# Performance work log

Measured on AMD Instinct MI355X. Metric: run time of the kernel, lower is better.

## Reference

```python
import jax, jax.numpy as jnp
import numpy as np
from jax import lax

B, T = 8, 256
GRID = (8, 8, 8)
X, Y, Z = GRID
N = X * Y * Z            # 512 nodes
C_IN = C_OUT = 8         # 4096 / 512
R = 8                    # num_rand


def _stencil_mask():
    # 7-point stencil mask at kernel center (1,1,1)
    m = np.zeros((3, 3, 3), dtype=np.float32)
    c = 1
    m[c, c, c] = 1.0
    m[c - 1, c, c] = 1.0
    m[c + 1, c, c] = 1.0
    m[c, c - 1, c] = 1.0
    m[c, c + 1, c] = 1.0
    m[c, c, c - 1] = 1.0
    m[c, c, c + 1] = 1.0
    return jnp.asarray(m)


def setup_inputs() -> dict:
    key = jax.random.key(0)
    k1, k2, k3, k4 = jax.random.split(key, 4)
    x = jax.random.normal(k1, (B, T, C_IN * N), dtype=jnp.float32)
    # MaskedConv3d params (kernel 3x3x3)
    fan = C_IN * 27
    conv_w = jax.random.normal(k2, (C_OUT, C_IN, 3, 3, 3), dtype=jnp.float32) / np.sqrt(fan)
    conv_b = jnp.zeros((C_OUT,), dtype=jnp.float32)
    # RandomGraphMixer3D params (xavier-uniform-like)
    bound = np.sqrt(6.0 / (C_IN * R + C_OUT))
    mix_w = jax.random.uniform(k3, (C_OUT, C_IN, R), jnp.float32, -bound, bound)
    mix_b = jnp.zeros((C_OUT,), dtype=jnp.float32)
    rand_indices = jax.random.randint(k4, (N, R), 0, N, dtype=jnp.int32)
    alpha = jnp.float32(0.5)
    return {"x": x, "conv_w": conv_w, "conv_b": conv_b,
            "mix_w": mix_w, "mix_b": mix_b, "alpha": alpha,
            "rand_indices": rand_indices}


def reference(x, conv_w, conv_b, mix_w, mix_b, alpha, rand_indices):
    Bd, Td, D = x.shape
    xt = x.reshape(Bd * Td, C_IN, X, Y, Z)
    # --- masked 7-point stencil conv3d ---
    w = conv_w * _stencil_mask()  # broadcast over (O, I)
    y_local = lax.conv_general_dilated(
        xt, w, window_strides=(1, 1, 1), padding='SAME',
        dimension_numbers=('NCDHW', 'OIDHW', 'NCDHW'))
    y_local = y_local + conv_b[None, :, None, None, None]
    # --- random graph mixer: gather + contract ---
    x_nodes = xt.reshape(Bd * Td, C_IN, N)
    gathered = x_nodes[:, :, rand_indices]              # [BT, C, N, R]
    y_rand = jnp.einsum('ocr,bcnr->bon', mix_w, gathered) + mix_b[None, :, None]
    y_rand = y_rand.reshape(Bd * Td, C_OUT, X, Y, Z)
    # --- sigmoid blend ---
    a = jax.nn.sigmoid(alpha)
    yt = a * y_local + (1.0 - a) * y_rand
    return yt.reshape(Bd, Td, C_OUT * N)
```

## Files before the change

kernel.cpp:

```cpp
#include <hip/hip_runtime.h>
#include <math.h>

#define NNODES 512
#define CIN 8
#define COUT 8
#define RR 8
#define BTB 2
#define GUARD 64
#define SLOTS (GUARD + NNODES + GUARD)
#define SLAB_HW (SLOTS * 8)
#define LDS_HW (BTB * SLAB_HW)
#define WTAB 1024

typedef __attribute__((ext_vector_type(8))) short short8;
typedef __attribute__((ext_vector_type(4))) float floatx4;

__device__ __forceinline__ unsigned int pack_bf16(float a, float b) {
    unsigned int ua = __float_as_uint(a);
    unsigned int ub = __float_as_uint(b);
    ua = (ua + 0x7fffu + ((ua >> 16) & 1u)) >> 16;
    ub = (ub + 0x7fffu + ((ub >> 16) & 1u)) & 0xffff0000u;
    return ua | ub;
}

__global__ void prep(const float* __restrict__ conv_w,
                     const float* __restrict__ conv_b,
                     const float* __restrict__ mix_w,
                     const float* __restrict__ mix_b,
                     const float* __restrict__ alpha_p,
                     const int*   __restrict__ rand_idx,
                     float* __restrict__ ws) {
    const int t = threadIdx.x;
    const float a = 1.0f / (1.0f + expf(-alpha_p[0]));
    if (t < 960) {
        const int oc = t / 15;
        const int tap = t % 15;
        float v;
        if (tap < 7) {
            const int off[7] = {13, 4, 22, 10, 16, 12, 14};
            v = a * conv_w[oc * 27 + off[tap]];
        } else {
            v = (1.0f - a) * mix_w[oc * RR + (tap - 7)];
        }
        ws[t] = v;
    } else if (t < 968) {
        const int o = t - 960;
        ws[960 + o] = a * conv_b[o] + (1.0f - a) * mix_b[o];
    }

    int4* tab = (int4*)((int*)ws + WTAB);
    for (int e = t; e < 2048; e += 1024) {
        const int tt = e >> 6, lane = e & 63;
        const int q = lane >> 4, r16 = lane & 15;
        const int m = tt * 16 + r16;
        const int h = (m >> 3) & 7, w = m & 7;
        int off[4];
#pragma unroll
        for (int i = 0; i < 4; ++i) {
            const int tap = 4 * i + q;
            int o;
            if (tap == 0)       o = GUARD + m;
            else if (tap == 1)  o = GUARD + m - 64;
            else if (tap == 2)  o = GUARD + m + 64;
            else if (tap == 3)  o = (h > 0) ? (GUARD + m - 8) : 0;
            else if (tap == 4)  o = (h < 7) ? (GUARD + m + 8) : 0;
            else if (tap == 5)  o = (w > 0) ? (GUARD + m - 1) : 0;
            else if (tap == 6)  o = (w < 7) ? (GUARD + m + 1) : 0;
            else if (tap <= 14) o = GUARD + rand_idx[m * RR + (tap - 7)];
            else                o = 0;
            off[i] = o * 16;
        }
        tab[e] = make_int4(off[0], off[1], off[2], off[3]);
    }
}

__global__ __launch_bounds__(256) void hybrid3d_v3(
    const float* __restrict__ x,
    const float* __restrict__ wsb,
    float* __restrict__ out)
{
    __shared__ unsigned short lds16[LDS_HW];
    const int tid  = threadIdx.x;
    const int wave = tid >> 6;
    const int lane = tid & 63;
    const int quad = lane >> 4;
    const int r16  = lane & 15;
    const int btl  = wave >> 1;
    const int half = wave & 1;

    {
        const int b = tid >> 7;
        const int s = tid & 127;
        const int slot = (s < GUARD) ? s : (NNODES + s);
        *(uint4*)&lds16[b * SLAB_HW + slot * 8] = make_uint4(0u, 0u, 0u, 0u);
    }

    short8 bfrag[4];
#pragma unroll
    for (int i = 0; i < 4; ++i) {
        const int tap = 4 * i + quad;
        union { unsigned int u[4]; short8 s; } bf;
#pragma unroll
        for (int jp = 0; jp < 4; ++jp) {
            const int c0 = 2 * jp, c1 = 2 * jp + 1;
            float f0 = (r16 < 8 && tap < 15) ? wsb[(r16 * CIN + c0) * 15 + tap] : 0.0f;
            float f1 = (r16 < 8 && tap < 15) ? wsb[(r16 * CIN + c1) * 15 + tap] : 0.0f;
            bf.u[jp] = pack_bf16(f0, f1);
        }
        bfrag[i] = bf.s;
    }
    const float bias = (r16 < 8) ? wsb[960 + r16] : 0.0f;

    const float* xg = x + ((size_t)blockIdx.x * BTB + btl) * (CIN * NNODES);
    unsigned short* slab = lds16 + btl * SLAB_HW;
#pragma unroll
    for (int j = 0; j < 4; ++j) {
        const int n = half * 256 + j * 64 + lane;
        float v[8];
#pragma unroll
        for (int c = 0; c < 8; ++c) v[c] = xg[c * NNODES + n];
        uint4 pk;
        pk.x = pack_bf16(v[0], v[1]);
        pk.y = pack_bf16(v[2], v[3]);
        pk.z = pack_bf16(v[4], v[5]);
        pk.w = pack_bf16(v[6], v[7]);
        *(uint4*)&slab[(GUARD + n) * 8] = pk;
    }
    __syncthreads();

    const char* slabp = (const char*)slab;
    const int4* tab = (const int4*)((const int*)wsb + WTAB);
    float* outb = out + ((size_t)blockIdx.x * BTB + btl) * (COUT * NNODES);

#pragma unroll 2
    for (int tt = 0; tt < 16; ++tt) {
        const int t = half * 16 + tt;
        const int4 off = tab[t * 64 + lane];
        union { uint4 u; short8 s; } r0, r1, r2, r3;
        r0.u = *(const uint4*)(slabp + off.x);
        r1.u = *(const uint4*)(slabp + off.y);
        r2.u = *(const uint4*)(slabp + off.z);
        r3.u = *(const uint4*)(slabp + off.w);

        floatx4 acc_a = {bias, bias, bias, bias};
        floatx4 acc_b = {0.0f, 0.0f, 0.0f, 0.0f};
        acc_a = __builtin_amdgcn_mfma_f32_16x16x32_bf16(r0.s, bfrag[0], acc_a, 0, 0, 0);
        acc_b = __builtin_amdgcn_mfma_f32_16x16x32_bf16(r2.s, bfrag[2], acc_b, 0, 0, 0);
        acc_a = __builtin_amdgcn_mfma_f32_16x16x32_bf16(r1.s, bfrag[1], acc_a, 0, 0, 0);
        acc_b = __builtin_amdgcn_mfma_f32_16x16x32_bf16(r3.s, bfrag[3], acc_b, 0, 0, 0);

        if (r16 < 8) {
            float4 res;
            res.x = acc_a.x + acc_b.x;
            res.y = acc_a.y + acc_b.y;
            res.z = acc_a.z + acc_b.z;
            res.w = acc_a.w + acc_b.w;
            *(float4*)(outb + r16 * NNODES + t * 16 + quad * 4) = res;
        }
    }
}

extern "C" void kernel_launch(void* const* d_in, const int* in_sizes, int n_in,
                              void* d_out, int out_size, void* d_ws, size_t ws_size,
                              hipStream_t stream) {
    const float* x       = (const float*)d_in[0];
    const float* conv_w  = (const float*)d_in[1];
    const float* conv_b  = (const float*)d_in[2];
    const float* mix_w   = (const float*)d_in[3];
    const float* mix_b   = (const float*)d_in[4];
    const float* alpha_p = (const float*)d_in[5];
    const int*   rand_i  = (const int*)d_in[6];
    float* out = (float*)d_out;
    float* ws  = (float*)d_ws;

    const int BT = in_sizes[0] / (CIN * NNODES);

    prep<<<1, 1024, 0, stream>>>(conv_w, conv_b, mix_w, mix_b, alpha_p, rand_i, ws);
    hybrid3d_v3<<<BT / BTB, 256, 0, stream>>>(x, ws, out);
}
```

Baseline: 105.0 us.

## Fuse weight-prep kernel into main kernel and compute gather offsets inline

```diff
diff --git a/kernel.cpp b/kernel.cpp
--- a/kernel.cpp
+++ b/kernel.cpp
@@ -10,7 +10,6 @@
 #define SLOTS (GUARD + NNODES + GUARD)
 #define SLAB_HW (SLOTS * 8)
 #define LDS_HW (BTB * SLAB_HW)
-#define WTAB 1024
 
 typedef __attribute__((ext_vector_type(8))) short short8;
 typedef __attribute__((ext_vector_type(4))) float floatx4;
@@ -23,63 +22,19 @@
     return ua | ub;
 }
 
-__global__ void prep(const float* __restrict__ conv_w,
-                     const float* __restrict__ conv_b,
-                     const float* __restrict__ mix_w,
-                     const float* __restrict__ mix_b,
-                     const float* __restrict__ alpha_p,
-                     const int*   __restrict__ rand_idx,
-                     float* __restrict__ ws) {
-    const int t = threadIdx.x;
-    const float a = 1.0f / (1.0f + expf(-alpha_p[0]));
-    if (t < 960) {
-        const int oc = t / 15;
-        const int tap = t % 15;
-        float v;
-        if (tap < 7) {
-            const int off[7] = {13, 4, 22, 10, 16, 12, 14};
-            v = a * conv_w[oc * 27 + off[tap]];
-        } else {
-            v = (1.0f - a) * mix_w[oc * RR + (tap - 7)];
-        }
-        ws[t] = v;
-    } else if (t < 968) {
-        const int o = t - 960;
-        ws[960 + o] = a * conv_b[o] + (1.0f - a) * mix_b[o];
-    }
-
-    int4* tab = (int4*)((int*)ws + WTAB);
-    for (int e = t; e < 2048; e += 1024) {
-        const int tt = e >> 6, lane = e & 63;
-        const int q = lane >> 4, r16 = lane & 15;
-        const int m = tt * 16 + r16;
-        const int h = (m >> 3) & 7, w = m & 7;
-        int off[4];
-#pragma unroll
-        for (int i = 0; i < 4; ++i) {
-            const int tap = 4 * i + q;
-            int o;
-            if (tap == 0)       o = GUARD + m;
-            else if (tap == 1)  o = GUARD + m - 64;
-            else if (tap == 2)  o = GUARD + m + 64;
-            else if (tap == 3)  o = (h > 0) ? (GUARD + m - 8) : 0;
-            else if (tap == 4)  o = (h < 7) ? (GUARD + m + 8) : 0;
-            else if (tap == 5)  o = (w > 0) ? (GUARD + m - 1) : 0;
-            else if (tap == 6)  o = (w < 7) ? (GUARD + m + 1) : 0;
-            else if (tap <= 14) o = GUARD + rand_idx[m * RR + (tap - 7)];
-            else                o = 0;
-            off[i] = o * 16;
-        }
-        tab[e] = make_int4(off[0], off[1], off[2], off[3]);
-    }
-}
-
-__global__ __launch_bounds__(256) void hybrid3d_v3(
+__global__ __launch_bounds__(256) void hybrid3d_v4(
     const float* __restrict__ x,
-    const float* __restrict__ wsb,
+    const float* __restrict__ conv_w,
+    const float* __restrict__ conv_b,
+    const float* __restrict__ mix_w,
+    const float* __restrict__ mix_b,
+    const float* __restrict__ alpha_p,
+    const int*   __restrict__ rand_idx,
     float* __restrict__ out)
 {
     __shared__ unsigned short lds16[LDS_HW];
+    float* wfold = (float*)lds16;
+
     const int tid  = threadIdx.x;
     const int wave = tid >> 6;
     const int lane = tid & 63;
@@ -88,12 +43,25 @@
     const int btl  = wave >> 1;
     const int half = wave & 1;
 
-    {
-        const int b = tid >> 7;
-        const int s = tid & 127;
-        const int slot = (s < GUARD) ? s : (NNODES + s);
-        *(uint4*)&lds16[b * SLAB_HW + slot * 8] = make_uint4(0u, 0u, 0u, 0u);
+    const float a = 1.0f / (1.0f + expf(-alpha_p[0]));
+
+    if (tid < 64) {
+        const float* cw = conv_w + tid * 27;
+        const float* mw = mix_w + tid * RR;
+        float* wf = wfold + tid * 15;
+        wf[0] = a * cw[13];
+        wf[1] = a * cw[4];
+        wf[2] = a * cw[22];
+        wf[3] = a * cw[10];
+        wf[4] = a * cw[16];
+        wf[5] = a * cw[12];
+        wf[6] = a * cw[14];
+        const float oma = 1.0f - a;
+#pragma unroll
+        for (int r = 0; r < RR; ++r) wf[7 + r] = oma * mw[r];
     }
+    const float bias = (r16 < 8) ? (a * conv_b[r16] + (1.0f - a) * mix_b[r16]) : 0.0f;
+    __syncthreads();
 
     short8 bfrag[4];
 #pragma unroll
@@ -103,14 +71,20 @@
 #pragma unroll
         for (int jp = 0; jp < 4; ++jp) {
             const int c0 = 2 * jp, c1 = 2 * jp + 1;
-            float f0 = (r16 < 8 && tap < 15) ? wsb[(r16 * CIN + c0) * 15 + tap] : 0.0f;
-            float f1 = (r16 < 8 && tap < 15) ? wsb[(r16 * CIN + c1) * 15 + tap] : 0.0f;
+            float f0 = (r16 < 8 && tap < 15) ? wfold[(r16 * CIN + c0) * 15 + tap] : 0.0f;
+            float f1 = (r16 < 8 && tap < 15) ? wfold[(r16 * CIN + c1) * 15 + tap] : 0.0f;
             bf.u[jp] = pack_bf16(f0, f1);
         }
         bfrag[i] = bf.s;
     }
-    const float bias = (r16 < 8) ? wsb[960 + r16] : 0.0f;
+    __syncthreads();
 
+    {
+        const int b = tid >> 7;
+        const int s = tid & 127;
+        const int slot = (s < GUARD) ? s : (NNODES + s);
+        *(uint4*)&lds16[b * SLAB_HW + slot * 8] = make_uint4(0u, 0u, 0u, 0u);
+    }
     const float* xg = x + ((size_t)blockIdx.x * BTB + btl) * (CIN * NNODES);
     unsigned short* slab = lds16 + btl * SLAB_HW;
 #pragma unroll
@@ -129,18 +103,41 @@
     __syncthreads();
 
     const char* slabp = (const char*)slab;
-    const int4* tab = (const int4*)((const int*)wsb + WTAB);
     float* outb = out + ((size_t)blockIdx.x * BTB + btl) * (COUT * NNODES);
+
+    const int  rA   = (quad + 1) & 3;
+    const bool q3f  = (quad == 3);
+    const bool isq0 = (quad == 0);
+    const int c0q = (quad == 0) ? 0 : (quad == 1) ? -1024 : (quad == 2) ? 1024 : -128;
+    const int c1q = (quad == 0) ? 128 : (quad == 1) ? -16 : 16;
+    const int w   = r16 & 7;
+    const bool p1w = (quad == 1) ? (w > 0) : (quad == 2) ? (w < 7) : false;
+    const int* rrow = rand_idx + rA;
 
 #pragma unroll 2
     for (int tt = 0; tt < 16; ++tt) {
         const int t = half * 16 + tt;
-        const int4 off = tab[t * 64 + lane];
+        const int m = t * 16 + r16;
+        const int hh = (m >> 3) & 7;
+        const int base = 1024 + m * 16;
+
+        const int gA = rrow[m * RR];
+        const int gB = rrow[m * RR + 4];
+        const int offA = 1024 + gA * 16;
+        const int offB = 1024 + gB * 16;
+
+        const bool p0 = (!q3f) || (hh > 0);
+        const int off0 = p0 ? (base + c0q) : 0;
+        const bool p1 = isq0 ? (hh < 7) : p1w;
+        const int off1 = q3f ? offA : (p1 ? (base + c1q) : 0);
+        const int off2 = q3f ? offB : offA;
+        const int off3 = q3f ? 0 : offB;
+
         union { uint4 u; short8 s; } r0, r1, r2, r3;
-        r0.u = *(const uint4*)(slabp + off.x);
-        r1.u = *(const uint4*)(slabp + off.y);
-        r2.u = *(const uint4*)(slabp + off.z);
-        r3.u = *(const uint4*)(slabp + off.w);
+        r0.u = *(const uint4*)(slabp + off0);
+        r1.u = *(const uint4*)(slabp + off1);
+        r2.u = *(const uint4*)(slabp + off2);
+        r3.u = *(const uint4*)(slabp + off3);
 
         floatx4 acc_a = {bias, bias, bias, bias};
         floatx4 acc_b = {0.0f, 0.0f, 0.0f, 0.0f};
@@ -171,10 +168,9 @@
     const float* alpha_p = (const float*)d_in[5];
     const int*   rand_i  = (const int*)d_in[6];
     float* out = (float*)d_out;
-    float* ws  = (float*)d_ws;
 
     const int BT = in_sizes[0] / (CIN * NNODES);
 
-    prep<<<1, 1024, 0, stream>>>(conv_w, conv_b, mix_w, mix_b, alpha_p, rand_i, ws);
-    hybrid3d_v3<<<BT / BTB, 256, 0, stream>>>(x, ws, out);
+    hybrid3d_v4<<<BT / BTB, 256, 0, stream>>>(x, conv_w, conv_b, mix_w, mix_b,
+                                              alpha_p, rand_i, out);
 }
```

New measurement: 106.0 us. Within noise of the previous version (+1.0%).
